# Kernel tuning notes

Measured on AMD Instinct MI355X. Metric: run time of the kernel, lower is better.

Reference implementation:

```python
import jax, jax.numpy as jnp
import numpy as np

HEADS = 8
D_K = 64
LN_EPS = 1e-6


def setup_inputs() -> dict:
    key = jax.random.key(0)
    ks = jax.random.split(key, 12)
    B, S, D = 4, 2048, 512
    inp = {
        "key": jax.random.normal(ks[0], (B, S, D), jnp.float32),
        "value": jax.random.normal(ks[1], (B, S, D), jnp.float32),
        "query": jax.random.normal(ks[2], (B, S, D), jnp.float32),
        "mask": jax.random.randint(ks[3], (B, S, S), 0, 2).astype(bool),
        # projection weights (torch Linear: y = x @ W.T + b)
        "Wk": jax.random.normal(ks[4], (D, D), jnp.float32) * (1.0 / np.sqrt(D)),
        "bk": jnp.zeros((D,), jnp.float32),
        "Wv": jax.random.normal(ks[5], (D, D), jnp.float32) * (1.0 / np.sqrt(D)),
        "bv": jnp.zeros((D,), jnp.float32),
        "Wq": jax.random.normal(ks[6], (D, D), jnp.float32) * (1.0 / np.sqrt(D)),
        "bq": jnp.zeros((D,), jnp.float32),
        # LayerNorm gain/bias
        "a2": jnp.ones((D,), jnp.float32),
        "b2": jnp.zeros((D,), jnp.float32),
    }
    return inp


def _attention(key, value, query, mask, Wk, bk, Wv, bv, Wq, bq, a2, b2):
    B, Sq, D = query.shape
    Sk = key.shape[1]
    H, dk = HEADS, D_K

    def split_heads(x, W, b):
        y = x @ W.T + b                                   # [B, S, D]
        return y.reshape(x.shape[0], x.shape[1], H, dk).transpose(0, 2, 1, 3)  # [B,H,S,dk]

    k_up = split_heads(key, Wk, bk)
    v_up = split_heads(value, Wv, bv)
    q_up = split_heads(query, Wq, bq)

    # scaled dot-product scores, full [B,H,Sq,Sk] matrix (as in the original bmm)
    scores = jnp.einsum("bhqd,bhkd->bhqk", q_up, k_up) / jnp.sqrt(jnp.asarray(dk, scores_dtype(q_up)))
    scores = jnp.where(mask[:, None, :, :], -jnp.inf, scores)
    attn = jax.nn.softmax(scores, axis=-1)                # dropout p=0 -> identity

    out = jnp.einsum("bhqk,bhkd->bhqd", attn, v_up)       # [B,H,Sq,dk]
    out = out.transpose(0, 2, 1, 3).reshape(B, Sq, D)
    res = out + query                                     # residual (res_dropout p=0)

    # OpenNMT LayerNorm: (x - mu) / (std + eps) * a2 + b2, unbiased std
    mu = res.mean(axis=-1, keepdims=True)
    var = jnp.sum((res - mu) ** 2, axis=-1, keepdims=True) / (D - 1)
    res = a2 * (res - mu) / (jnp.sqrt(var) + LN_EPS) + b2

    attn_flat = attn.reshape(B * H, Sq, Sk)               # matches torch [B*H, Sq, Sk]
    return res, attn_flat


def scores_dtype(x):
    return x.dtype


def reference(key, value, query, mask, Wk, bk, Wv, bv, Wq, bq, a2, b2):
    return _attention(key, value, query, mask, Wk, bk, Wv, bv, Wq, bq, a2, b2)
```

## Files before the change

kernel.cpp:

```cpp
#include <hip/hip_runtime.h>
#include <stdint.h>

typedef float f32x4 __attribute__((ext_vector_type(4)));
typedef short bf16x8 __attribute__((ext_vector_type(8)));

constexpr int NB = 4;
constexpr int NS = 2048;
constexpr int ND = 512;
constexpr int NH = 8;
constexpr int NDK = 64;
constexpr int NT = NS / 64;

static __device__ __forceinline__ unsigned short f2bf(float f) {
    union { float f; uint32_t u; } v; v.f = f;
    uint32_t r = (v.u + 0x7FFFu + ((v.u >> 16) & 1u)) >> 16;
    return (unsigned short)r;
}
static __device__ __forceinline__ unsigned short f2bf_fast(float f) {
    union { float f; uint32_t u; } v; v.f = f;
    return (unsigned short)((v.u + 0x8000u) >> 16);
}

static __device__ __forceinline__ void gload_lds16(const void* g, void* l) {
    __builtin_amdgcn_global_load_lds((const __attribute__((address_space(1))) void*)g,
                                     (__attribute__((address_space(3))) void*)l, 16, 0, 0);
}

__global__ __launch_bounds__(256) void cvt3_kernel(const float4* __restrict__ a,
                                                   const float4* __restrict__ b,
                                                   const float4* __restrict__ c,
                                                   ushort4* __restrict__ oa,
                                                   ushort4* __restrict__ ob,
                                                   ushort4* __restrict__ oc, int n4) {
    int which = blockIdx.y;
    const float4* in = which == 0 ? a : which == 1 ? b : c;
    ushort4* out = which == 0 ? oa : which == 1 ? ob : oc;
    int i = blockIdx.x * blockDim.x + threadIdx.x;
    if (i >= n4) return;
    float4 v = in[i];
    ushort4 o;
    o.x = f2bf(v.x); o.y = f2bf(v.y); o.z = f2bf(v.z); o.w = f2bf(v.w);
    out[i] = o;
}

__global__ __launch_bounds__(256) void bitmask_kernel(const int* __restrict__ mask,
                                                      unsigned long long* __restrict__ bm,
                                                      int nwords) {
    int lane = threadIdx.x & 63;
    int wave = threadIdx.x >> 6;
    int wgid = blockIdx.x * 4 + wave;
    int nw = gridDim.x * 4;
    for (int c = wgid; c < nwords; c += nw) {
        int v = mask[(size_t)c * 64 + lane];
        unsigned long long bits = __ballot(v != 0);
        if (lane == 0) bm[c] = bits;
    }
}

__global__ __launch_bounds__(256) void proj_kernel(const unsigned short* __restrict__ xq,
                                                   const unsigned short* __restrict__ xk,
                                                   const unsigned short* __restrict__ xv,
                                                   const unsigned short* __restrict__ wq,
                                                   const unsigned short* __restrict__ wk,
                                                   const unsigned short* __restrict__ wv,
                                                   const float* __restrict__ bq,
                                                   const float* __restrict__ bk,
                                                   const float* __restrict__ bv,
                                                   unsigned short* __restrict__ Qw,
                                                   unsigned short* __restrict__ Kw,
                                                   unsigned short* __restrict__ VTw) {
    int z = blockIdx.z;
    const unsigned short* X = z == 0 ? xq : z == 1 ? xk : xv;
    const unsigned short* W = z == 0 ? wq : z == 1 ? wk : wv;
    const float* bias = z == 0 ? bq : z == 1 ? bk : bv;
    unsigned short* out = z == 0 ? Qw : z == 1 ? Kw : VTw;
    float scale = z == 0 ? 0.125f : 1.0f;
    int vtrans = (z == 2);

    int lane = threadIdx.x & 63;
    int wave = threadIdx.x >> 6;
    int lrow = lane & 15, lgrp = lane >> 4;
    int m0 = blockIdx.x * 64 + wave * 16;
    int n0 = blockIdx.y * 64;

    f32x4 acc[4] = {{0.f,0.f,0.f,0.f},{0.f,0.f,0.f,0.f},{0.f,0.f,0.f,0.f},{0.f,0.f,0.f,0.f}};
    const unsigned short* xrow = X + (size_t)(m0 + lrow) * ND;
    for (int k = 0; k < ND; k += 32) {
        bf16x8 a = *(const bf16x8*)(xrow + k + lgrp * 8);
#pragma unroll
        for (int n = 0; n < 4; n++) {
            bf16x8 b = *(const bf16x8*)(W + (size_t)(n0 + n * 16 + lrow) * ND + k + lgrp * 8);
            acc[n] = __builtin_amdgcn_mfma_f32_16x16x32_bf16(a, b, acc[n], 0, 0, 0);
        }
    }
#pragma unroll
    for (int n = 0; n < 4; n++) {
        int col = n0 + n * 16 + lrow;
        int h = col >> 6, d = col & 63;
        float bv_ = bias[col];
#pragma unroll
        for (int j = 0; j < 4; j++) {
            int m = m0 + lgrp * 4 + j;
            int bidx = m >> 11, s = m & (NS - 1);
            float y = (acc[n][j] + bv_) * scale;
            size_t off = vtrans ? ((size_t)(bidx * NH + h) * NDK + d) * NS + s
                                : ((size_t)(bidx * NH + h) * NS + s) * NDK + d;
            out[off] = f2bf(y);
        }
    }
}

__global__ __launch_bounds__(512) void attn_kernel(const unsigned short* __restrict__ Q,
                                                   const unsigned short* __restrict__ K,
                                                   const unsigned short* __restrict__ VT,
                                                   const unsigned long long* __restrict__ bm,
                                                   float* __restrict__ attn_out,
                                                   float* __restrict__ Ob) {
    __shared__ __align__(16) unsigned short kb[2][64 * 64];
    __shared__ __align__(16) unsigned short vb[2][64 * 64];
    __shared__ __align__(16) unsigned short pl[8][16][80];

    int lane = threadIdx.x & 63;
    int wave = threadIdx.x >> 6;
    int lrow = lane & 15, lgrp = lane >> 4;

    int id = blockIdx.x;
    int xcd = id & 7;
    int loc = id >> 3;
    int bh = xcd * 4 + (loc >> 4);
    int qb = loc & 15;
    int b = bh >> 3, h = bh & 7;
    int qbase = qb * 128;
    int qw = qbase + wave * 16;

    const unsigned short* qrow = Q + ((size_t)bh * NS + qw + lrow) * NDK + lgrp * 8;
    bf16x8 aq0 = *(const bf16x8*)(qrow);
    bf16x8 aq1 = *(const bf16x8*)(qrow + 32);

    const unsigned short* kbase = K + (size_t)bh * NS * NDK;
    const unsigned short* vbase = VT + (size_t)bh * NDK * NS;
    const unsigned long long* bmb = bm + (size_t)b * NS * (NS / 64);
    int bmoff[4];
#pragma unroll
    for (int j = 0; j < 4; j++) bmoff[j] = (qw + lgrp * 4 + j) * (NS / 64);

    int rl = lane >> 3, cc = lane & 7;
    int cs = (cc ^ rl) * 8;

    {
        const unsigned short* s0 = kbase + (size_t)(8 * wave + rl) * NDK + cs;
        gload_lds16(s0, &kb[0][wave * 512]);
    }
    __syncthreads();

    float lacc[4] = {0.f, 0.f, 0.f, 0.f};
    for (int t = 0; t < NT; t++) {
        int buf = t & 1;
        if (t + 1 < NT) {
            const unsigned short* s0 = kbase + (size_t)((t + 1) * 64 + 8 * wave + rl) * NDK + cs;
            gload_lds16(s0, &kb[buf ^ 1][wave * 512]);
        }
        f32x4 sc[4] = {{0.f,0.f,0.f,0.f},{0.f,0.f,0.f,0.f},{0.f,0.f,0.f,0.f},{0.f,0.f,0.f,0.f}};
#pragma unroll
        for (int n = 0; n < 4; n++) {
            int R = n * 16 + lrow;
            bf16x8 b0 = *(const bf16x8*)&kb[buf][R * 64 + ((lgrp ^ (lrow & 7)) * 8)];
            bf16x8 b1 = *(const bf16x8*)&kb[buf][R * 64 + (((4 + lgrp) ^ (lrow & 7)) * 8)];
            sc[n] = __builtin_amdgcn_mfma_f32_16x16x32_bf16(aq0, b0, sc[n], 0, 0, 0);
            sc[n] = __builtin_amdgcn_mfma_f32_16x16x32_bf16(aq1, b1, sc[n], 0, 0, 0);
        }
        unsigned long long w[4];
#pragma unroll
        for (int j = 0; j < 4; j++) w[j] = bmb[bmoff[j] + t];
#pragma unroll
        for (int n = 0; n < 4; n++)
#pragma unroll
            for (int j = 0; j < 4; j++) {
                float e = __expf(sc[n][j]);
                lacc[j] += ((w[j] >> (n * 16 + lrow)) & 1) ? 0.f : e;
            }
        __syncthreads();
    }
    float invl[4];
#pragma unroll
    for (int j = 0; j < 4; j++) {
        float l = lacc[j];
        l += __shfl_xor(l, 1);
        l += __shfl_xor(l, 2);
        l += __shfl_xor(l, 4);
        l += __shfl_xor(l, 8);
        invl[j] = 1.f / l;
    }

    {
        const unsigned short* s0 = kbase + (size_t)(8 * wave + rl) * NDK + cs;
        gload_lds16(s0, &kb[0][wave * 512]);
        const unsigned short* s1 = vbase + (size_t)(8 * wave + rl) * NS + cs;
        gload_lds16(s1, &vb[0][wave * 512]);
    }
    __syncthreads();

    f32x4 accO[4] = {{0.f,0.f,0.f,0.f},{0.f,0.f,0.f,0.f},{0.f,0.f,0.f,0.f},{0.f,0.f,0.f,0.f}};
    float* aout = attn_out + (size_t)bh * NS * NS;
    float* abase[4];
#pragma unroll
    for (int j = 0; j < 4; j++) abase[j] = aout + (size_t)(qw + lgrp * 4 + j) * NS + lrow;

    for (int t = 0; t < NT; t++) {
        int buf = t & 1;
        int kt = t * 64;
        if (t + 1 < NT) {
            const unsigned short* s0 = kbase + (size_t)((t + 1) * 64 + 8 * wave + rl) * NDK + cs;
            gload_lds16(s0, &kb[buf ^ 1][wave * 512]);
            const unsigned short* s1 = vbase + (size_t)(8 * wave + rl) * NS + (t + 1) * 64 + cs;
            gload_lds16(s1, &vb[buf ^ 1][wave * 512]);
        }
        f32x4 sc[4] = {{0.f,0.f,0.f,0.f},{0.f,0.f,0.f,0.f},{0.f,0.f,0.f,0.f},{0.f,0.f,0.f,0.f}};
#pragma unroll
        for (int n = 0; n < 4; n++) {
            int R = n * 16 + lrow;
            bf16x8 b0 = *(const bf16x8*)&kb[buf][R * 64 + ((lgrp ^ (lrow & 7)) * 8)];
            bf16x8 b1 = *(const bf16x8*)&kb[buf][R * 64 + (((4 + lgrp) ^ (lrow & 7)) * 8)];
            sc[n] = __builtin_amdgcn_mfma_f32_16x16x32_bf16(aq0, b0, sc[n], 0, 0, 0);
            sc[n] = __builtin_amdgcn_mfma_f32_16x16x32_bf16(aq1, b1, sc[n], 0, 0, 0);
        }
        unsigned long long w[4];
#pragma unroll
        for (int j = 0; j < 4; j++) w[j] = bmb[bmoff[j] + t];
#pragma unroll
        for (int n = 0; n < 4; n++)
#pragma unroll
            for (int j = 0; j < 4; j++) {
                float e = ((w[j] >> (n * 16 + lrow)) & 1) ? 0.f : __expf(sc[n][j]);
                abase[j][kt + n * 16] = e * invl[j];
                pl[wave][lgrp * 4 + j][n * 16 + lrow] = f2bf_fast(e);
            }
#pragma unroll
        for (int step = 0; step < 2; step++) {
            bf16x8 ap = *(const bf16x8*)&pl[wave][lrow][step * 32 + lgrp * 8];
#pragma unroll
            for (int n = 0; n < 4; n++) {
                int R = n * 16 + lrow;
                bf16x8 bv = *(const bf16x8*)&vb[buf][R * 64 + (((4 * step + lgrp) ^ (lrow & 7)) * 8)];
                accO[n] = __builtin_amdgcn_mfma_f32_16x16x32_bf16(ap, bv, accO[n], 0, 0, 0);
            }
        }
        __syncthreads();
    }

#pragma unroll
    for (int n = 0; n < 4; n++)
#pragma unroll
        for (int j = 0; j < 4; j++) {
            int qi = qw + lgrp * 4 + j;
            Ob[((size_t)b * NS + qi) * ND + h * NDK + n * 16 + lrow] = accO[n][j] * invl[j];
        }
}

__global__ __launch_bounds__(256) void ln_kernel(const float* __restrict__ Ob,
                                                 const float* __restrict__ query,
                                                 const float* __restrict__ a2,
                                                 const float* __restrict__ b2,
                                                 float* __restrict__ out) {
    int row = blockIdx.x * 4 + (threadIdx.x >> 6);
    int lane = threadIdx.x & 63;
    const float4* orow = (const float4*)(Ob + (size_t)row * ND);
    const float4* qrow = (const float4*)(query + (size_t)row * ND);
    float4 v[2];
    float sum = 0.f;
#pragma unroll
    for (int t = 0; t < 2; t++) {
        float4 o = orow[lane + t * 64];
        float4 q = qrow[lane + t * 64];
        v[t].x = o.x + q.x; v[t].y = o.y + q.y; v[t].z = o.z + q.z; v[t].w = o.w + q.w;
        sum += v[t].x + v[t].y + v[t].z + v[t].w;
    }
#pragma unroll
    for (int s = 1; s < 64; s <<= 1) sum += __shfl_xor(sum, s);
    float mu = sum * (1.f / ND);
    float sq = 0.f;
#pragma unroll
    for (int t = 0; t < 2; t++) {
        float dx = v[t].x - mu, dy = v[t].y - mu, dz = v[t].z - mu, dw = v[t].w - mu;
        sq += dx * dx + dy * dy + dz * dz + dw * dw;
    }
#pragma unroll
    for (int s = 1; s < 64; s <<= 1) sq += __shfl_xor(sq, s);
    float var = sq * (1.f / (ND - 1));
    float inv = 1.f / (sqrtf(var) + 1e-6f);
    float4* orow_out = (float4*)(out + (size_t)row * ND);
#pragma unroll
    for (int t = 0; t < 2; t++) {
        float4 g = ((const float4*)a2)[lane + t * 64];
        float4 bb = ((const float4*)b2)[lane + t * 64];
        float4 r;
        r.x = g.x * (v[t].x - mu) * inv + bb.x;
        r.y = g.y * (v[t].y - mu) * inv + bb.y;
        r.z = g.z * (v[t].z - mu) * inv + bb.z;
        r.w = g.w * (v[t].w - mu) * inv + bb.w;
        orow_out[lane + t * 64] = r;
    }
}

extern "C" void kernel_launch(void* const* d_in, const int* in_sizes, int n_in,
                              void* d_out, int out_size, void* d_ws, size_t ws_size,
                              hipStream_t stream) {
    const float* key   = (const float*)d_in[0];
    const float* value = (const float*)d_in[1];
    const float* query = (const float*)d_in[2];
    const int*   mask  = (const int*)d_in[3];
    const float* Wk = (const float*)d_in[4];
    const float* bk = (const float*)d_in[5];
    const float* Wv = (const float*)d_in[6];
    const float* bv = (const float*)d_in[7];
    const float* Wq = (const float*)d_in[8];
    const float* bq = (const float*)d_in[9];
    const float* a2 = (const float*)d_in[10];
    const float* b2 = (const float*)d_in[11];

    const size_t nX = (size_t)NB * NS * ND;
    const size_t nW = (size_t)ND * ND;
    const int    nBMw = NB * NS * NS / 64;

    unsigned short* xq  = (unsigned short*)d_ws;
    unsigned short* xk  = xq + nX;
    unsigned short* xv  = xk + nX;
    unsigned short* wqb = xv + nX;
    unsigned short* wkb = wqb + nW;
    unsigned short* wvb = wkb + nW;
    unsigned short* Qw  = wvb + nW;
    unsigned short* Kw  = Qw + nX;
    unsigned short* VTw = Kw + nX;
    float* Ow = (float*)(VTw + nX);
    unsigned long long* bmw = (unsigned long long*)(Ow + nX);

    bitmask_kernel<<<2048, 256, 0, stream>>>(mask, bmw, nBMw);

    cvt3_kernel<<<dim3((int)(nX / 4 / 256), 3), 256, 0, stream>>>(
        (const float4*)query, (const float4*)key, (const float4*)value,
        (ushort4*)xq, (ushort4*)xk, (ushort4*)xv, (int)(nX / 4));
    cvt3_kernel<<<dim3((int)(nW / 4 / 256), 3), 256, 0, stream>>>(
        (const float4*)Wq, (const float4*)Wk, (const float4*)Wv,
        (ushort4*)wqb, (ushort4*)wkb, (ushort4*)wvb, (int)(nW / 4));

    proj_kernel<<<dim3(128, 8, 3), 256, 0, stream>>>(xq, xk, xv, wqb, wkb, wvb,
                                                     bq, bk, bv, Qw, Kw, VTw);

    float* attn_out = (float*)d_out + nX;
    attn_kernel<<<512, 512, 0, stream>>>(Qw, Kw, VTw, bmw, attn_out, Ow);

    ln_kernel<<<2048, 256, 0, stream>>>(Ow, query, a2, b2, (float*)d_out);
}
```

Before: 387.4 us.

## Fold log2e into Q scale, prefetch mask words, defer attn stores, add setprio

```diff
diff --git a/kernel.cpp b/kernel.cpp
--- a/kernel.cpp
+++ b/kernel.cpp
@@ -10,6 +10,7 @@
 constexpr int NH = 8;
 constexpr int NDK = 64;
 constexpr int NT = NS / 64;
+constexpr float QSCALE = 0.125f * 1.44269504088896340736f;
 
 static __device__ __forceinline__ unsigned short f2bf(float f) {
     union { float f; uint32_t u; } v; v.f = f;
@@ -19,6 +20,13 @@
 static __device__ __forceinline__ unsigned short f2bf_fast(float f) {
     union { float f; uint32_t u; } v; v.f = f;
     return (unsigned short)((v.u + 0x8000u) >> 16);
+}
+static __device__ __forceinline__ float exp2_fast(float x) {
+#if __has_builtin(__builtin_amdgcn_exp2f)
+    return __builtin_amdgcn_exp2f(x);
+#else
+    return exp2f(x);
+#endif
 }
 
 static __device__ __forceinline__ void gload_lds16(const void* g, void* l) {
@@ -74,7 +82,7 @@
     const unsigned short* W = z == 0 ? wq : z == 1 ? wk : wv;
     const float* bias = z == 0 ? bq : z == 1 ? bk : bv;
     unsigned short* out = z == 0 ? Qw : z == 1 ? Kw : VTw;
-    float scale = z == 0 ? 0.125f : 1.0f;
+    float scale = z == 0 ? QSCALE : 1.0f;
     int vtrans = (z == 2);
 
     int lane = threadIdx.x & 63;
@@ -130,8 +138,7 @@
     int bh = xcd * 4 + (loc >> 4);
     int qb = loc & 15;
     int b = bh >> 3, h = bh & 7;
-    int qbase = qb * 128;
-    int qw = qbase + wave * 16;
+    int qw = qb * 128 + wave * 16;
 
     const unsigned short* qrow = Q + ((size_t)bh * NS + qw + lrow) * NDK + lgrp * 8;
     bf16x8 aq0 = *(const bf16x8*)(qrow);
@@ -151,16 +158,24 @@
         const unsigned short* s0 = kbase + (size_t)(8 * wave + rl) * NDK + cs;
         gload_lds16(s0, &kb[0][wave * 512]);
     }
+    unsigned long long wc[4], wn[4];
+#pragma unroll
+    for (int j = 0; j < 4; j++) wc[j] = bmb[bmoff[j]];
     __syncthreads();
 
     float lacc[4] = {0.f, 0.f, 0.f, 0.f};
     for (int t = 0; t < NT; t++) {
         int buf = t & 1;
+        int tn = (t + 1 < NT) ? t + 1 : t;
         if (t + 1 < NT) {
-            const unsigned short* s0 = kbase + (size_t)((t + 1) * 64 + 8 * wave + rl) * NDK + cs;
+            const unsigned short* s0 = kbase + (size_t)(tn * 64 + 8 * wave + rl) * NDK + cs;
             gload_lds16(s0, &kb[buf ^ 1][wave * 512]);
         }
+#pragma unroll
+        for (int j = 0; j < 4; j++) wn[j] = bmb[bmoff[j] + tn];
+
         f32x4 sc[4] = {{0.f,0.f,0.f,0.f},{0.f,0.f,0.f,0.f},{0.f,0.f,0.f,0.f},{0.f,0.f,0.f,0.f}};
+        __builtin_amdgcn_s_setprio(1);
 #pragma unroll
         for (int n = 0; n < 4; n++) {
             int R = n * 16 + lrow;
@@ -169,19 +184,22 @@
             sc[n] = __builtin_amdgcn_mfma_f32_16x16x32_bf16(aq0, b0, sc[n], 0, 0, 0);
             sc[n] = __builtin_amdgcn_mfma_f32_16x16x32_bf16(aq1, b1, sc[n], 0, 0, 0);
         }
-        unsigned long long w[4];
-#pragma unroll
-        for (int j = 0; j < 4; j++) w[j] = bmb[bmoff[j] + t];
-#pragma unroll
-        for (int n = 0; n < 4; n++)
-#pragma unroll
-            for (int j = 0; j < 4; j++) {
-                float e = __expf(sc[n][j]);
-                lacc[j] += ((w[j] >> (n * 16 + lrow)) & 1) ? 0.f : e;
+        __builtin_amdgcn_s_setprio(0);
+#pragma unroll
+        for (int j = 0; j < 4; j++) {
+            uint32_t wlo = (uint32_t)wc[j], whi = (uint32_t)(wc[j] >> 32);
+#pragma unroll
+            for (int n = 0; n < 4; n++) {
+                uint32_t bit = ((n < 2 ? wlo : whi) >> ((n & 1) * 16 + lrow)) & 1u;
+                float e = exp2_fast(sc[n][j]);
+                lacc[j] += bit ? 0.f : e;
             }
+        }
+#pragma unroll
+        for (int j = 0; j < 4; j++) wc[j] = wn[j];
         __syncthreads();
     }
-    float invl[4];
+    float li[4];
 #pragma unroll
     for (int j = 0; j < 4; j++) {
         float l = lacc[j];
@@ -189,7 +207,7 @@
         l += __shfl_xor(l, 2);
         l += __shfl_xor(l, 4);
         l += __shfl_xor(l, 8);
-        invl[j] = 1.f / l;
+        li[j] = -__log2f(l);
     }
 
     {
@@ -198,6 +216,8 @@
         const unsigned short* s1 = vbase + (size_t)(8 * wave + rl) * NS + cs;
         gload_lds16(s1, &vb[0][wave * 512]);
     }
+#pragma unroll
+    for (int j = 0; j < 4; j++) wc[j] = bmb[bmoff[j]];
     __syncthreads();
 
     f32x4 accO[4] = {{0.f,0.f,0.f,0.f},{0.f,0.f,0.f,0.f},{0.f,0.f,0.f,0.f},{0.f,0.f,0.f,0.f}};
@@ -206,16 +226,29 @@
 #pragma unroll
     for (int j = 0; j < 4; j++) abase[j] = aout + (size_t)(qw + lgrp * 4 + j) * NS + lrow;
 
+    float pst[4][4];
     for (int t = 0; t < NT; t++) {
         int buf = t & 1;
-        int kt = t * 64;
+        int tn = (t + 1 < NT) ? t + 1 : t;
+        if (t > 0) {
+            int ktp = (t - 1) * 64;
+#pragma unroll
+            for (int n = 0; n < 4; n++)
+#pragma unroll
+                for (int j = 0; j < 4; j++)
+                    abase[j][ktp + n * 16] = pst[n][j];
+        }
         if (t + 1 < NT) {
-            const unsigned short* s0 = kbase + (size_t)((t + 1) * 64 + 8 * wave + rl) * NDK + cs;
+            const unsigned short* s0 = kbase + (size_t)(tn * 64 + 8 * wave + rl) * NDK + cs;
             gload_lds16(s0, &kb[buf ^ 1][wave * 512]);
-            const unsigned short* s1 = vbase + (size_t)(8 * wave + rl) * NS + (t + 1) * 64 + cs;
+            const unsigned short* s1 = vbase + (size_t)(8 * wave + rl) * NS + tn * 64 + cs;
             gload_lds16(s1, &vb[buf ^ 1][wave * 512]);
         }
+#pragma unroll
+        for (int j = 0; j < 4; j++) wn[j] = bmb[bmoff[j] + tn];
+
         f32x4 sc[4] = {{0.f,0.f,0.f,0.f},{0.f,0.f,0.f,0.f},{0.f,0.f,0.f,0.f},{0.f,0.f,0.f,0.f}};
+        __builtin_amdgcn_s_setprio(1);
 #pragma unroll
         for (int n = 0; n < 4; n++) {
             int R = n * 16 + lrow;
@@ -224,17 +257,19 @@
             sc[n] = __builtin_amdgcn_mfma_f32_16x16x32_bf16(aq0, b0, sc[n], 0, 0, 0);
             sc[n] = __builtin_amdgcn_mfma_f32_16x16x32_bf16(aq1, b1, sc[n], 0, 0, 0);
         }
-        unsigned long long w[4];
-#pragma unroll
-        for (int j = 0; j < 4; j++) w[j] = bmb[bmoff[j] + t];
-#pragma unroll
-        for (int n = 0; n < 4; n++)
-#pragma unroll
-            for (int j = 0; j < 4; j++) {
-                float e = ((w[j] >> (n * 16 + lrow)) & 1) ? 0.f : __expf(sc[n][j]);
-                abase[j][kt + n * 16] = e * invl[j];
-                pl[wave][lgrp * 4 + j][n * 16 + lrow] = f2bf_fast(e);
+        __builtin_amdgcn_s_setprio(0);
+#pragma unroll
+        for (int j = 0; j < 4; j++) {
+            uint32_t wlo = (uint32_t)wc[j], whi = (uint32_t)(wc[j] >> 32);
+#pragma unroll
+            for (int n = 0; n < 4; n++) {
+                uint32_t bit = ((n < 2 ? wlo : whi) >> ((n & 1) * 16 + lrow)) & 1u;
+                float p = bit ? 0.f : exp2_fast(sc[n][j] + li[j]);
+                pst[n][j] = p;
+                pl[wave][lgrp * 4 + j][n * 16 + lrow] = f2bf_fast(p);
             }
+        }
+        __builtin_amdgcn_s_setprio(1);
 #pragma unroll
         for (int step = 0; step < 2; step++) {
             bf16x8 ap = *(const bf16x8*)&pl[wave][lrow][step * 32 + lgrp * 8];
@@ -245,7 +280,18 @@
                 accO[n] = __builtin_amdgcn_mfma_f32_16x16x32_bf16(ap, bv, accO[n], 0, 0, 0);
             }
         }
+        __builtin_amdgcn_s_setprio(0);
+#pragma unroll
+        for (int j = 0; j < 4; j++) wc[j] = wn[j];
         __syncthreads();
+    }
+    {
+        int ktp = (NT - 1) * 64;
+#pragma unroll
+        for (int n = 0; n < 4; n++)
+#pragma unroll
+            for (int j = 0; j < 4; j++)
+                abase[j][ktp + n * 16] = pst[n][j];
     }
 
 #pragma unroll
@@ -253,7 +299,7 @@
 #pragma unroll
         for (int j = 0; j < 4; j++) {
             int qi = qw + lgrp * 4 + j;
-            Ob[((size_t)b * NS + qi) * ND + h * NDK + n * 16 + lrow] = accO[n][j] * invl[j];
+            Ob[((size_t)b * NS + qi) * ND + h * NDK + n * 16 + lrow] = accO[n][j];
         }
 }
 
```

After: 397.9 us. 2.7% more time.
